# Kernel tuning notes

Measured on AMD Instinct MI355X. Metric: run time of the kernel, lower is better.

Reference implementation:

```python
import jax, jax.numpy as jnp
import numpy as np

DIM = 2048
N_HEADS = 16
N_KV_HEADS = 8
HEAD_DIM = DIM // N_HEADS  # 128
N_REP = N_HEADS // N_KV_HEADS  # 2
HIDDEN = 4 * DIM  # Project hidden dim
SEQ = 2048
BSZ = 2
ROPE_THETA = 10000.0
NEG_INF = -1e9


def setup_inputs() -> dict:
    key = jax.random.key(0)
    ks = jax.random.split(key, 10)
    s_in = 1.0 / np.sqrt(DIM)
    s_hid = 1.0 / np.sqrt(HIDDEN)
    x = jax.random.normal(ks[0], (BSZ, SEQ, DIM), jnp.float32)
    wq = jax.random.normal(ks[1], (DIM, N_HEADS * HEAD_DIM), jnp.float32) * s_in
    wk_w1 = jax.random.normal(ks[2], (DIM, HIDDEN), jnp.float32) * s_in
    wk_w2 = jax.random.normal(ks[3], (HIDDEN, N_KV_HEADS * HEAD_DIM), jnp.float32) * s_hid
    wk_w3 = jax.random.normal(ks[4], (DIM, HIDDEN), jnp.float32) * s_in
    wv_w1 = jax.random.normal(ks[5], (DIM, HIDDEN), jnp.float32) * s_in
    wv_w2 = jax.random.normal(ks[6], (HIDDEN, N_KV_HEADS * HEAD_DIM), jnp.float32) * s_hid
    wv_w3 = jax.random.normal(ks[7], (DIM, HIDDEN), jnp.float32) * s_in
    wo = jax.random.normal(ks[8], (N_HEADS * HEAD_DIM, DIM), jnp.float32) * s_in
    # RoPE tables: angle[t, j] = t * theta^(-2j/head_dim), j in [0, head_dim/2)
    inv_freq = 1.0 / (ROPE_THETA ** (np.arange(0, HEAD_DIM, 2, dtype=np.float64) / HEAD_DIM))
    ang = np.outer(np.arange(SEQ, dtype=np.float64), inv_freq)
    freqs_cos = jnp.asarray(np.cos(ang), jnp.float32)  # [SEQ, HEAD_DIM//2]
    freqs_sin = jnp.asarray(np.sin(ang), jnp.float32)
    # causal additive mask [1, 1, SEQ, SEQ]
    mask = jnp.triu(jnp.full((SEQ, SEQ), NEG_INF, jnp.float32), k=1)[None, None]
    return {
        "x": x, "wq": wq,
        "wk_w1": wk_w1, "wk_w2": wk_w2, "wk_w3": wk_w3,
        "wv_w1": wv_w1, "wv_w2": wv_w2, "wv_w3": wv_w3,
        "wo": wo, "freqs_cos": freqs_cos, "freqs_sin": freqs_sin,
        "mask": mask, "start_pos": 0,
    }


def _rope(x, cos, sin):
    # x: [b, s, h, d]; pairs (x[2j], x[2j+1]) rotated as complex multiply
    xr = x[..., 0::2]
    xi = x[..., 1::2]
    c = cos[None, :, None, :]
    s = sin[None, :, None, :]
    out_r = xr * c - xi * s
    out_i = xr * s + xi * c
    return jnp.stack([out_r, out_i], axis=-1).reshape(x.shape)


def _project(x, w1, w2, w3):
    # SwiGLU-style projection: w2(silu(x@w1) * (x@w3))
    return (jax.nn.silu(x @ w1) * (x @ w3)) @ w2


def reference(x, wq, wk_w1, wk_w2, wk_w3, wv_w1, wv_w2, wv_w3, wo,
              freqs_cos, freqs_sin, mask, start_pos):
    b, s, _ = x.shape
    q = (x @ wq).reshape(b, s, N_HEADS, HEAD_DIM)
    q = _rope(q, freqs_cos, freqs_sin)
    k = _project(x, wk_w1, wk_w2, wk_w3).reshape(b, s, N_KV_HEADS, HEAD_DIM)
    v = _project(x, wv_w1, wv_w2, wv_w3).reshape(b, s, N_KV_HEADS, HEAD_DIM)
    k = _rope(k, freqs_cos, freqs_sin)
    o_keys, o_values = k, v  # is_training=True path: cache is just current k/v
    # repeat_kv (GQA) -> [b, h, s, d]
    kr = jnp.repeat(k, N_REP, axis=2).transpose(0, 2, 1, 3)
    vr = jnp.repeat(v, N_REP, axis=2).transpose(0, 2, 1, 3)
    qt = q.transpose(0, 2, 1, 3)
    scores = jnp.einsum('bhqd,bhkd->bhqk', qt, kr) / np.sqrt(HEAD_DIM).astype(np.float32)
    scores = scores + mask
    attn = jax.nn.softmax(scores.astype(jnp.float32), axis=-1).astype(qt.dtype)
    out = jnp.einsum('bhqk,bhkd->bhqd', attn, vr)
    out = out.transpose(0, 2, 1, 3).reshape(b, s, N_HEADS * HEAD_DIM)
    return (out @ wo, o_keys, o_values)
```

## Files before the change

kernel.cpp:

```cpp
#include <hip/hip_runtime.h>

typedef unsigned short ushort_t;
typedef __attribute__((ext_vector_type(4))) float f32x4;
typedef __attribute__((ext_vector_type(8))) __bf16 bf16x8;
typedef __attribute__((ext_vector_type(4))) unsigned short ushort4_t;
typedef __attribute__((ext_vector_type(8))) unsigned short ushort8_t;
typedef __attribute__((ext_vector_type(2))) unsigned int u32x2;

#define AS1 __attribute__((address_space(1)))
#define AS3 __attribute__((address_space(3)))

__device__ __forceinline__ float bf2f(ushort_t u) {
  unsigned int v = ((unsigned int)u) << 16;
  return __builtin_bit_cast(float, v);
}
__device__ __forceinline__ ushort_t f2bf(float f) {
  unsigned int u = __builtin_bit_cast(unsigned int, f);
  u += 0x7fffu + ((u >> 16) & 1u);
  return (ushort_t)(u >> 16);
}
__device__ __forceinline__ void storeC(float* p, float v) { *p = v; }
__device__ __forceinline__ void storeC(ushort_t* p, float v) { *p = f2bf(v); }

__global__ __launch_bounds__(256) void cast_f32_bf16(const float* __restrict__ in,
                                                     ushort_t* __restrict__ outp) {
  size_t i = ((size_t)blockIdx.x * 256 + threadIdx.x) * 4;
  f32x4 v = *(const f32x4*)(const void*)&in[i];
  ushort4_t o;
#pragma unroll
  for (int j = 0; j < 4; ++j) o[j] = f2bf(v[j]);
  *(ushort4_t*)(void*)&outp[i] = o;
}

__global__ __launch_bounds__(256) void transpose_cast_b(
    const float* __restrict__ W0, const float* __restrict__ W1,
    const float* __restrict__ W2, const float* __restrict__ W3,
    ushort_t* __restrict__ Wt, int K, int N, long long strT) {
  __shared__ float tile[32][33];
  const int z = blockIdx.z;
  const float* W = (z == 0) ? W0 : (z == 1) ? W1 : (z == 2) ? W2 : W3;
  ushort_t* out = Wt + (size_t)(strT * z);
  int n0 = blockIdx.x * 32, k0 = blockIdx.y * 32;
  int tx = threadIdx.x, ty = threadIdx.y;
#pragma unroll
  for (int i = 0; i < 4; ++i)
    tile[ty + 8 * i][tx] = W[(size_t)(k0 + ty + 8 * i) * N + n0 + tx];
  __syncthreads();
#pragma unroll
  for (int i = 0; i < 4; ++i)
    out[(size_t)(n0 + ty + 8 * i) * K + k0 + tx] = f2bf(tile[tx][ty + 8 * i]);
}

__global__ __launch_bounds__(256) void silu_mul(ushort_t* __restrict__ h1,
                                                const ushort_t* __restrict__ h3) {
  size_t i = ((size_t)blockIdx.x * 256 + threadIdx.x) * 8;
  ushort8_t a = *(const ushort8_t*)(const void*)&h1[i];
  ushort8_t b = *(const ushort8_t*)(const void*)&h3[i];
#pragma unroll
  for (int j = 0; j < 8; ++j) {
    float x = bf2f(a[j]);
    float g = x / (1.0f + __expf(-x));
    a[j] = f2bf(g * bf2f(b[j]));
  }
  *(ushort8_t*)(void*)&h1[i] = a;
}

__global__ __launch_bounds__(256) void reduce_q(const ushort_t* __restrict__ part,
                                                ushort_t* __restrict__ qb,
                                                const float* __restrict__ fc,
                                                const float* __restrict__ fs) {
  const float alpha = 0.08838834764831845f;
  int p = blockIdx.x * 256 + threadIdx.x;
  size_t e0 = (size_t)p * 8;
  int i0 = (int)((e0 & 127) >> 1);
  int s = (int)((e0 >> 11) & 2047);
  ushort8_t a = *(const ushort8_t*)(const void*)&part[e0];
  ushort8_t b = *(const ushort8_t*)(const void*)&part[e0 + 8388608];
  f32x4 c4 = *(const f32x4*)(const void*)&fc[s * 64 + i0];
  f32x4 s4 = *(const f32x4*)(const void*)&fs[s * 64 + i0];
  ushort8_t o;
#pragma unroll
  for (int j = 0; j < 4; ++j) {
    float xr = bf2f(a[2 * j]) + bf2f(b[2 * j]);
    float xi = bf2f(a[2 * j + 1]) + bf2f(b[2 * j + 1]);
    float c = c4[j] * alpha, sn = s4[j] * alpha;
    o[2 * j] = f2bf(xr * c - xi * sn);
    o[2 * j + 1] = f2bf(xr * sn + xi * c);
  }
  *(ushort8_t*)(void*)&qb[e0] = o;
}

__global__ __launch_bounds__(256) void reduce_k(const ushort_t* __restrict__ part,
                                                ushort_t* __restrict__ kb,
                                                float* __restrict__ okeys,
                                                const float* __restrict__ fc,
                                                const float* __restrict__ fs) {
  int p = blockIdx.x * 256 + threadIdx.x;
  size_t e0 = (size_t)p * 8;
  int i0 = (int)((e0 & 127) >> 1);
  int s = (int)((e0 >> 10) & 2047);
  ushort8_t a0 = *(const ushort8_t*)(const void*)&part[e0];
  ushort8_t a1 = *(const ushort8_t*)(const void*)&part[e0 + 4194304];
  ushort8_t a2 = *(const ushort8_t*)(const void*)&part[e0 + 8388608];
  ushort8_t a3 = *(const ushort8_t*)(const void*)&part[e0 + 12582912];
  f32x4 c4 = *(const f32x4*)(const void*)&fc[s * 64 + i0];
  f32x4 s4 = *(const f32x4*)(const void*)&fs[s * 64 + i0];
  ushort8_t o;
  f32x4 ov0, ov1;
#pragma unroll
  for (int j = 0; j < 4; ++j) {
    float xr = bf2f(a0[2 * j]) + bf2f(a1[2 * j]) + bf2f(a2[2 * j]) + bf2f(a3[2 * j]);
    float xi = bf2f(a0[2 * j + 1]) + bf2f(a1[2 * j + 1]) + bf2f(a2[2 * j + 1]) +
               bf2f(a3[2 * j + 1]);
    float c = c4[j], sn = s4[j];
    float orr = xr * c - xi * sn;
    float oi = xr * sn + xi * c;
    o[2 * j] = f2bf(orr);
    o[2 * j + 1] = f2bf(oi);
    if (j < 2) { ov0[2 * j] = orr; ov0[2 * j + 1] = oi; }
    else       { ov1[2 * (j - 2)] = orr; ov1[2 * (j - 2) + 1] = oi; }
  }
  *(ushort8_t*)(void*)&kb[e0] = o;
  *(f32x4*)(void*)&okeys[e0] = ov0;
  *(f32x4*)(void*)&okeys[e0 + 4] = ov1;
}

__global__ __launch_bounds__(256) void reduce_v(const ushort_t* __restrict__ part,
                                                float* __restrict__ ovals,
                                                ushort_t* __restrict__ vbT) {
  __shared__ ushort_t tile[32][33];
  int s0 = blockIdx.x * 32, d0 = blockIdx.y * 32, bk = blockIdx.z;
  int b = bk >> 3, kh = bk & 7;
  int tx = threadIdx.x, ty = threadIdx.y;
#pragma unroll
  for (int i = 0; i < 4; ++i) {
    int s = s0 + ty + 8 * i;
    size_t src = ((size_t)(b * 2048 + s)) * 1024 + kh * 128 + d0 + tx;
    float v = bf2f(part[src]) + bf2f(part[src + 4194304]) +
              bf2f(part[src + 8388608]) + bf2f(part[src + 12582912]);
    tile[ty + 8 * i][tx] = f2bf(v);
    ovals[src] = v;
  }
  __syncthreads();
#pragma unroll
  for (int i = 0; i < 4; ++i) {
    int d = d0 + ty + 8 * i;
    vbT[((size_t)bk * 128 + d) * 2048 + s0 + tx] = tile[tx][ty + 8 * i];
  }
}

__global__ __launch_bounds__(256) void reduce_wo(const float* __restrict__ part,
                                                 float* __restrict__ outp) {
  size_t i = ((size_t)blockIdx.x * 256 + threadIdx.x) * 4;
  f32x4 a = *(const f32x4*)(const void*)&part[i];
  f32x4 b = *(const f32x4*)(const void*)&part[i + 8388608];
  *(f32x4*)(void*)&outp[i] = a + b;
}

__global__ __launch_bounds__(256) void flash_attn(
    const ushort_t* __restrict__ Q, const ushort_t* __restrict__ Kg,
    const ushort_t* __restrict__ VT, ushort_t* __restrict__ O) {
  __shared__ __align__(16) char smem[81920];
  const int xp = blockIdx.x;
  const int bh = blockIdx.y;
  const int b = bh >> 4, h = bh & 15, kh = h >> 1;
  const int t = threadIdx.x, w = t >> 6, lane = t & 63;
  const int fr = lane & 15, fh = lane >> 4;
  const size_t kelem0 = ((size_t)b * 2048) * 1024 + kh * 128;
  const size_t velem0 = ((size_t)(b * 8 + kh)) * 128 * 2048;
  const size_t qrow0 = (size_t)b * 2048;

  size_t oK[4], oV[4];
#pragma unroll
  for (int qv = 0; qv < 4; ++qv) {
    int row = w * 16 + qv * 4 + (lane >> 4);
    oK[qv] = (size_t)row * 1024 + (((lane & 15) ^ (row & 7)) * 8);
    int rd = w * 32 + qv * 8 + (lane >> 3);
    oV[qv] = (size_t)rd * 2048 + (((lane & 7) ^ (rd & 7)) * 8);
  }

  auto stage = [&](int tile, int buf) {
    const size_t kc = (size_t)tile * 64 * 1024;
    const int vc = tile * 64;
    char* kd = smem + buf * 16384 + w * 4096;
    char* vd = smem + 32768 + buf * 16384 + w * 4096;
#pragma unroll
    for (int qv = 0; qv < 4; ++qv) {
      __builtin_amdgcn_global_load_lds((const AS1 void*)(Kg + kelem0 + kc + oK[qv]),
                                       (AS3 void*)(kd + qv * 1024), 16, 0, 0);
      __builtin_amdgcn_global_load_lds((const AS1 void*)(VT + velem0 + oV[qv] + vc),
                                       (AS3 void*)(vd + qv * 1024), 16, 0, 0);
    }
  };

#pragma unroll 1
  for (int ph = 0; ph < 2; ++ph) {
    const int qi = ph ? (15 - xp) : xp;
    const int qw = qi * 128 + w * 32;
    const int nt = 2 * qi + 2;

    bf16x8 qF[2][4];
#pragma unroll
    for (int qt = 0; qt < 2; ++qt)
#pragma unroll
      for (int i = 0; i < 4; ++i)
        qF[qt][i] = *(const bf16x8*)(const void*)(
            Q + (qrow0 + qw + qt * 16 + fr) * 2048 + h * 128 + i * 32 + fh * 8);

    f32x4 acco[8][2] = {};
    float mrun[2] = {-1e30f, -1e30f};
    float lrun[2] = {0.0f, 0.0f};

    stage(0, 0);
#pragma unroll 1
    for (int tt = 0; tt < nt; ++tt) {
      const int c0 = tt * 64;
      if (tt + 1 < nt) {
        stage(tt + 1, (tt + 1) & 1);
        asm volatile("s_waitcnt vmcnt(8)" ::: "memory");
      } else {
        asm volatile("s_waitcnt vmcnt(0)" ::: "memory");
      }
      __builtin_amdgcn_sched_barrier(0);
      __builtin_amdgcn_s_barrier();
      const char* KL = smem + (tt & 1) * 16384;
      const char* VL = smem + 32768 + (tt & 1) * 16384;
      char* PL = smem + 65536 + w * 4096;
      if (c0 <= qw + 31) {
        f32x4 sacc[2][4] = {};
#pragma unroll
        for (int i = 0; i < 4; ++i)
#pragma unroll
          for (int mt = 0; mt < 4; ++mt) {
            bf16x8 kf = *(const bf16x8*)(const void*)(
                KL + (mt * 16 + fr) * 256 + (((i * 4 + fh) ^ (fr & 7)) * 16));
            sacc[0][mt] = __builtin_amdgcn_mfma_f32_16x16x32_bf16(kf, qF[0][i], sacc[0][mt], 0, 0, 0);
            sacc[1][mt] = __builtin_amdgcn_mfma_f32_16x16x32_bf16(kf, qF[1][i], sacc[1][mt], 0, 0, 0);
          }
        if (c0 + 63 > qw) {
#pragma unroll
          for (int qt = 0; qt < 2; ++qt) {
            int qg = qw + qt * 16 + fr;
#pragma unroll
            for (int mt = 0; mt < 4; ++mt)
#pragma unroll
              for (int j = 0; j < 4; ++j)
                if (c0 + mt * 16 + fh * 4 + j > qg) sacc[qt][mt][j] = -1e30f;
          }
        }
#pragma unroll
        for (int qt = 0; qt < 2; ++qt) {
          float mt_ = -1e30f;
#pragma unroll
          for (int mt = 0; mt < 4; ++mt)
#pragma unroll
            for (int j = 0; j < 4; ++j) mt_ = fmaxf(mt_, sacc[qt][mt][j]);
          mt_ = fmaxf(mt_, __shfl_xor(mt_, 16, 64));
          mt_ = fmaxf(mt_, __shfl_xor(mt_, 32, 64));
          float mnew = fmaxf(mrun[qt], mt_);
          float corr = __expf(mrun[qt] - mnew);
          mrun[qt] = mnew;
          float ps = 0.0f;
          float pv[4][4];
#pragma unroll
          for (int mt = 0; mt < 4; ++mt)
#pragma unroll
            for (int j = 0; j < 4; ++j) {
              float pe = __expf(sacc[qt][mt][j] - mnew);
              pv[mt][j] = pe;
              ps += pe;
            }
          ps += __shfl_xor(ps, 16, 64);
          ps += __shfl_xor(ps, 32, 64);
          lrun[qt] = lrun[qt] * corr + ps;
#pragma unroll
          for (int mt = 0; mt < 4; ++mt) {
            unsigned int u0, u1;
            asm("v_cvt_pk_bf16_f32 %0, %1, %2" : "=v"(u0) : "v"(pv[mt][0]), "v"(pv[mt][1]));
            asm("v_cvt_pk_bf16_f32 %0, %1, %2" : "=v"(u1) : "v"(pv[mt][2]), "v"(pv[mt][3]));
            u32x2 val;
            val[0] = u0;
            val[1] = u1;
            *(u32x2*)(void*)(PL + qt * 2048 + fr * 128 +
                             (((2 * mt + (fh >> 1)) ^ (fr & 7)) * 16) + (fh & 1) * 8) = val;
          }
#pragma unroll
          for (int dt = 0; dt < 8; ++dt) acco[dt][qt] *= corr;
        }
        bf16x8 pf[2][2];
#pragma unroll
        for (int qt = 0; qt < 2; ++qt)
#pragma unroll
          for (int ks = 0; ks < 2; ++ks)
            pf[qt][ks] = *(const bf16x8*)(const void*)(
                PL + qt * 2048 + fr * 128 + (((ks * 4 + fh) ^ (fr & 7)) * 16));
#pragma unroll
        for (int dt = 0; dt < 8; ++dt)
#pragma unroll
          for (int ks = 0; ks < 2; ++ks) {
            bf16x8 vf = *(const bf16x8*)(const void*)(
                VL + (dt * 16 + fr) * 128 + (((ks * 4 + fh) ^ (fr & 7)) * 16));
            acco[dt][0] = __builtin_amdgcn_mfma_f32_16x16x32_bf16(vf, pf[0][ks], acco[dt][0], 0, 0, 0);
            acco[dt][1] = __builtin_amdgcn_mfma_f32_16x16x32_bf16(vf, pf[1][ks], acco[dt][1], 0, 0, 0);
          }
      }
      __builtin_amdgcn_s_barrier();
    }
#pragma unroll
    for (int qt = 0; qt < 2; ++qt) {
      float inv = 1.0f / lrun[qt];
      const size_t rb = (qrow0 + qw + qt * 16 + fr) * 2048 + h * 128;
#pragma unroll
      for (int dt = 0; dt < 8; ++dt) {
        ushort4_t o4;
#pragma unroll
        for (int j = 0; j < 4; ++j) o4[j] = f2bf(acco[dt][qt][j] * inv);
        *(ushort4_t*)(void*)(O + rb + dt * 16 + fh * 4) = o4;
      }
    }
  }
}

template <typename CT>
__global__ __launch_bounds__(512, 2) void gemm256(
    const ushort_t* __restrict__ A, const ushort_t* __restrict__ B,
    CT* __restrict__ C, int K, int lda, int ldb, int ldc,
    int nwgx, int nwg, long long strA, long long strB, long long strC) {
  __shared__ __align__(16) char smem[131072];
  const int bz = blockIdx.y;
  const int bid = blockIdx.x;
  const int swz = (bid & 7) * (nwg >> 3) + (bid >> 3);
  const int r0 = (swz / nwgx) * 256;
  const int c0 = (swz % nwgx) * 256;
  const int t = threadIdx.x, w = t >> 6, lane = t & 63;
  const int wm = w >> 2, wn = w & 3;
  const int fr = lane & 15, fh = lane >> 4;
  const int sl2 = (fh ^ ((fr >> 1) & 3)) << 4;
  const int ldsw = w * 1024;
  const int srow = t >> 2;
  const int scb = (t & 3) ^ ((srow >> 1) & 3);
  const int NT = K >> 5;
  const ushort_t* gA = A + strA * bz + (size_t)(r0 + srow) * lda + scb * 8;
  const ushort_t* gB = B + strB * bz + (size_t)(c0 + srow) * ldb + scb * 8;

  auto stage = [&](int tile, int h, int slot) {
    char* lp = (char*)smem + slot * 16384 + ldsw;
    __builtin_amdgcn_global_load_lds(
        (const AS1 void*)(gA + (size_t)(h * 128) * lda + tile * 32),
        (AS3 void*)lp, 16, 0, 0);
    __builtin_amdgcn_global_load_lds(
        (const AS1 void*)(gB + (size_t)(h * 128) * ldb + tile * 32),
        (AS3 void*)(lp + 8192), 16, 0, 0);
  };

  f32x4 acc[8][4] = {};

  stage(0, 0, 0); stage(0, 1, 1);
  if (NT > 1) { stage(1, 0, 2); stage(1, 1, 3); }
  if (NT > 2) { stage(2, 0, 4); stage(2, 1, 5); }
  if (NT > 2)
    asm volatile("s_waitcnt vmcnt(8)" ::: "memory");
  else if (NT > 1)
    asm volatile("s_waitcnt vmcnt(4)" ::: "memory");
  else
    asm volatile("s_waitcnt vmcnt(0)" ::: "memory");
  __builtin_amdgcn_sched_barrier(0);
  __builtin_amdgcn_s_barrier();
  __builtin_amdgcn_sched_barrier(0);

  int slA = wm;
  int slB = wn >> 1;
  int st0 = 6, st1 = 7;
  const int bQuart = 8192 + (wn & 1) * 4096;

  for (int kt = 0; kt < NT; ++kt) {
    const char* la = (const char*)smem + slA * 16384 + fr * 64 + sl2;
    const char* lb = (const char*)smem + slB * 16384 + bQuart + fr * 64 + sl2;
    bf16x8 aF[8], bF[4];
#pragma unroll
    for (int m = 0; m < 4; ++m)
      aF[m] = *(const bf16x8*)(const void*)(la + m * 1024);
#pragma unroll
    for (int n = 0; n < 4; ++n)
      bF[n] = *(const bf16x8*)(const void*)(lb + n * 1024);
#pragma unroll
    for (int m = 4; m < 8; ++m)
      aF[m] = *(const bf16x8*)(const void*)(la + m * 1024);
    if (kt + 3 < NT) { stage(kt + 3, 0, st0); stage(kt + 3, 1, st1); }
    __builtin_amdgcn_sched_barrier(0);
    __builtin_amdgcn_s_setprio(1);
#pragma unroll
    for (int m = 0; m < 4; ++m)
#pragma unroll
      for (int n = 0; n < 4; ++n)
        acc[m][n] = __builtin_amdgcn_mfma_f32_16x16x32_bf16(aF[m], bF[n], acc[m][n], 0, 0, 0);
#pragma unroll
    for (int m = 4; m < 8; ++m)
#pragma unroll
      for (int n = 0; n < 4; ++n)
        acc[m][n] = __builtin_amdgcn_mfma_f32_16x16x32_bf16(aF[m], bF[n], acc[m][n], 0, 0, 0);
    __builtin_amdgcn_s_setprio(0);
    if (kt + 1 < NT) {
      if (kt + 3 < NT)
        asm volatile("s_waitcnt vmcnt(8)" ::: "memory");
      else if (kt + 2 < NT)
        asm volatile("s_waitcnt vmcnt(4)" ::: "memory");
      else
        asm volatile("s_waitcnt vmcnt(0)" ::: "memory");
      __builtin_amdgcn_sched_barrier(0);
      __builtin_amdgcn_s_barrier();
      __builtin_amdgcn_sched_barrier(0);
    }
    slA = (slA + 2) & 7;
    slB = (slB + 2) & 7;
    st0 = (st0 + 2) & 7;
    st1 = (st1 + 2) & 7;
  }

  CT* gC = C + strC * bz;
  const int cr = r0 + wm * 128 + fh * 4;
  const int cc = c0 + wn * 64 + fr;
#pragma unroll
  for (int m = 0; m < 8; ++m)
#pragma unroll
    for (int n = 0; n < 4; ++n)
#pragma unroll
      for (int j = 0; j < 4; ++j)
        storeC(&gC[(size_t)(cr + m * 16 + j) * ldc + cc + n * 16], acc[m][n][j]);
}

extern "C" void kernel_launch(void* const* d_in, const int* in_sizes, int n_in,
                              void* d_out, int out_size, void* d_ws, size_t ws_size,
                              hipStream_t stream) {
  const float* x = (const float*)d_in[0];
  const float* wq = (const float*)d_in[1];
  const float* wk1 = (const float*)d_in[2];
  const float* wk2 = (const float*)d_in[3];
  const float* wk3 = (const float*)d_in[4];
  const float* wv1 = (const float*)d_in[5];
  const float* wv2 = (const float*)d_in[6];
  const float* wv3 = (const float*)d_in[7];
  const float* wo = (const float*)d_in[8];
  const float* fc = (const float*)d_in[9];
  const float* fs = (const float*)d_in[10];

  float* outp = (float*)d_out;
  float* okeys = outp + 8388608;
  float* ovals = outp + 12582912;

  char* p = (char*)d_ws;
  auto alloc = [&](size_t bytes) {
    char* r = p;
    p += (bytes + 255) & ~(size_t)255;
    return r;
  };
  ushort_t* xb = (ushort_t*)alloc(8388608ull * 2);
  ushort_t* w4T = (ushort_t*)alloc(4ull * 16777216 * 2);
  ushort_t* w2T = (ushort_t*)alloc(2ull * 8388608 * 2);
  ushort_t* wqoT = (ushort_t*)alloc(2ull * 4194304 * 2);
  ushort_t* qb = (ushort_t*)alloc(8388608ull * 2);
  ushort_t* kb = (ushort_t*)alloc(4194304ull * 2);
  ushort_t* vbT = (ushort_t*)alloc(4194304ull * 2);
  ushort_t* ob = (ushort_t*)alloc(8388608ull * 2);
  char* hreg = alloc(134217728ull);
  ushort_t* h1 = (ushort_t*)hreg;
  ushort_t* part16 = (ushort_t*)(hreg + 67108864);
  ushort_t* partQ16 = (ushort_t*)hreg;
  float* partWO = (float*)hreg;

  ushort_t* wk1T = w4T;
  ushort_t* wk2T = w2T;
  ushort_t* wv1T = w4T + 2ull * 16777216;
  ushort_t* wv2T = w2T + 8388608;
  ushort_t* wqT = wqoT;
  ushort_t* woT = wqoT + 4194304;

  dim3 tb(32, 8);

  cast_f32_bf16<<<8192, 256, 0, stream>>>(x, xb);
  transpose_cast_b<<<dim3(256, 64, 4), tb, 0, stream>>>(wk1, wk3, wv1, wv3, w4T,
                                                        2048, 8192, 16777216);
  transpose_cast_b<<<dim3(32, 256, 2), tb, 0, stream>>>(wk2, wv2, wk2, wv2, w2T,
                                                        8192, 1024, 8388608);
  transpose_cast_b<<<dim3(64, 64, 2), tb, 0, stream>>>(wq, wo, wq, wo, wqoT,
                                                       2048, 2048, 4194304);

  gemm256<ushort_t><<<dim3(128, 2), 512, 0, stream>>>(
      xb, wqT, partQ16, 1024, 2048, 2048, 2048, 8, 128, 1024, 1024, 8388608);
  reduce_q<<<4096, 256, 0, stream>>>(partQ16, qb, fc, fs);

  gemm256<ushort_t><<<dim3(512, 2), 512, 0, stream>>>(
      xb, wk1T, h1, 2048, 2048, 2048, 8192, 32, 512, 0, 16777216, 33554432);
  silu_mul<<<16384, 256, 0, stream>>>(h1, h1 + 33554432);
  gemm256<ushort_t><<<dim3(64, 4), 512, 0, stream>>>(
      h1, wk2T, part16, 2048, 8192, 8192, 1024, 4, 64, 2048, 2048, 4194304);
  reduce_k<<<2048, 256, 0, stream>>>(part16, kb, okeys, fc, fs);

  gemm256<ushort_t><<<dim3(512, 2), 512, 0, stream>>>(
      xb, wv1T, h1, 2048, 2048, 2048, 8192, 32, 512, 0, 16777216, 33554432);
  silu_mul<<<16384, 256, 0, stream>>>(h1, h1 + 33554432);
  gemm256<ushort_t><<<dim3(64, 4), 512, 0, stream>>>(
      h1, wv2T, part16, 2048, 8192, 8192, 1024, 4, 64, 2048, 2048, 4194304);
  reduce_v<<<dim3(64, 4, 16), tb, 0, stream>>>(part16, ovals, vbT);

  flash_attn<<<dim3(8, 32), 256, 0, stream>>>(qb, kb, vbT, ob);

  gemm256<float><<<dim3(128, 2), 512, 0, stream>>>(
      ob, woT, partWO, 1024, 2048, 2048, 2048, 8, 128, 1024, 1024, 8388608);
  reduce_wo<<<8192, 256, 0, stream>>>(partWO, outp);

  (void)in_sizes; (void)n_in; (void)out_size; (void)ws_size;
}
```

Baseline: 1.017 ms.

## Shrink GEMM tile to 128x256 with double-buffered LDS and higher occupancy

The shared GEMM kernel moves from a 256x256 tile with a 4-deep, 128KB LDS pipeline to a 128x256 tile with a simple two-buffer 48KB pipeline. Each wave now holds a 4x4 accumulator block, and launch bounds request 4 blocks per CU. Grids double to cover the smaller row tiles, and the split-K partial buffer for the K/V down-projection is moved into the transposed-weight workspace. The aim is to fit more workgroups per CU and more tiles per launch so more latency can be hidden. The cost is less data reuse per tile, a shallower prefetch, and a full vmcnt(0) wait every K step.

```diff
diff --git a/kernel.cpp b/kernel.cpp
--- a/kernel.cpp
+++ b/kernel.cpp
@@ -322,106 +322,82 @@
 }
 
 template <typename CT>
-__global__ __launch_bounds__(512, 2) void gemm256(
+__global__ __launch_bounds__(512, 4) void gemm256(
     const ushort_t* __restrict__ A, const ushort_t* __restrict__ B,
     CT* __restrict__ C, int K, int lda, int ldb, int ldc,
     int nwgx, int nwg, long long strA, long long strB, long long strC) {
-  __shared__ __align__(16) char smem[131072];
+  __shared__ __align__(16) char smem[49152];
   const int bz = blockIdx.y;
   const int bid = blockIdx.x;
   const int swz = (bid & 7) * (nwg >> 3) + (bid >> 3);
-  const int r0 = (swz / nwgx) * 256;
+  const int r0 = (swz / nwgx) * 128;
   const int c0 = (swz % nwgx) * 256;
   const int t = threadIdx.x, w = t >> 6, lane = t & 63;
   const int wm = w >> 2, wn = w & 3;
   const int fr = lane & 15, fh = lane >> 4;
   const int sl2 = (fh ^ ((fr >> 1) & 3)) << 4;
-  const int ldsw = w * 1024;
   const int srow = t >> 2;
   const int scb = (t & 3) ^ ((srow >> 1) & 3);
   const int NT = K >> 5;
   const ushort_t* gA = A + strA * bz + (size_t)(r0 + srow) * lda + scb * 8;
   const ushort_t* gB = B + strB * bz + (size_t)(c0 + srow) * ldb + scb * 8;
 
-  auto stage = [&](int tile, int h, int slot) {
-    char* lp = (char*)smem + slot * 16384 + ldsw;
+  auto stage = [&](int tile) {
+    const int buf = tile & 1;
     __builtin_amdgcn_global_load_lds(
-        (const AS1 void*)(gA + (size_t)(h * 128) * lda + tile * 32),
-        (AS3 void*)lp, 16, 0, 0);
+        (const AS1 void*)(gA + tile * 32),
+        (AS3 void*)((char*)smem + buf * 8192 + t * 16), 16, 0, 0);
     __builtin_amdgcn_global_load_lds(
-        (const AS1 void*)(gB + (size_t)(h * 128) * ldb + tile * 32),
-        (AS3 void*)(lp + 8192), 16, 0, 0);
+        (const AS1 void*)(gB + tile * 32),
+        (AS3 void*)((char*)smem + 16384 + buf * 16384 + t * 16), 16, 0, 0);
+    __builtin_amdgcn_global_load_lds(
+        (const AS1 void*)(gB + (size_t)128 * ldb + tile * 32),
+        (AS3 void*)((char*)smem + 16384 + buf * 16384 + 8192 + t * 16), 16, 0, 0);
   };
 
-  f32x4 acc[8][4] = {};
-
-  stage(0, 0, 0); stage(0, 1, 1);
-  if (NT > 1) { stage(1, 0, 2); stage(1, 1, 3); }
-  if (NT > 2) { stage(2, 0, 4); stage(2, 1, 5); }
-  if (NT > 2)
-    asm volatile("s_waitcnt vmcnt(8)" ::: "memory");
-  else if (NT > 1)
-    asm volatile("s_waitcnt vmcnt(4)" ::: "memory");
-  else
-    asm volatile("s_waitcnt vmcnt(0)" ::: "memory");
+  f32x4 acc[4][4] = {};
+
+  stage(0);
+  asm volatile("s_waitcnt vmcnt(0)" ::: "memory");
   __builtin_amdgcn_sched_barrier(0);
   __builtin_amdgcn_s_barrier();
   __builtin_amdgcn_sched_barrier(0);
 
-  int slA = wm;
-  int slB = wn >> 1;
-  int st0 = 6, st1 = 7;
-  const int bQuart = 8192 + (wn & 1) * 4096;
+  const int aBase = wm * 4096 + fr * 64 + sl2;
+  const int bBase = 16384 + wn * 4096 + fr * 64 + sl2;
 
   for (int kt = 0; kt < NT; ++kt) {
-    const char* la = (const char*)smem + slA * 16384 + fr * 64 + sl2;
-    const char* lb = (const char*)smem + slB * 16384 + bQuart + fr * 64 + sl2;
-    bf16x8 aF[8], bF[4];
+    if (kt + 1 < NT) stage(kt + 1);
+    const char* la = (const char*)smem + ((kt & 1) * 8192) + aBase;
+    const char* lb = (const char*)smem + ((kt & 1) * 16384) + bBase;
+    bf16x8 aF[4], bF[4];
 #pragma unroll
     for (int m = 0; m < 4; ++m)
       aF[m] = *(const bf16x8*)(const void*)(la + m * 1024);
 #pragma unroll
     for (int n = 0; n < 4; ++n)
       bF[n] = *(const bf16x8*)(const void*)(lb + n * 1024);
-#pragma unroll
-    for (int m = 4; m < 8; ++m)
-      aF[m] = *(const bf16x8*)(const void*)(la + m * 1024);
-    if (kt + 3 < NT) { stage(kt + 3, 0, st0); stage(kt + 3, 1, st1); }
     __builtin_amdgcn_sched_barrier(0);
     __builtin_amdgcn_s_setprio(1);
 #pragma unroll
     for (int m = 0; m < 4; ++m)
-#pragma unroll
-      for (int n = 0; n < 4; ++n)
-        acc[m][n] = __builtin_amdgcn_mfma_f32_16x16x32_bf16(aF[m], bF[n], acc[m][n], 0, 0, 0);
-#pragma unroll
-    for (int m = 4; m < 8; ++m)
 #pragma unroll
       for (int n = 0; n < 4; ++n)
         acc[m][n] = __builtin_amdgcn_mfma_f32_16x16x32_bf16(aF[m], bF[n], acc[m][n], 0, 0, 0);
     __builtin_amdgcn_s_setprio(0);
     if (kt + 1 < NT) {
-      if (kt + 3 < NT)
-        asm volatile("s_waitcnt vmcnt(8)" ::: "memory");
-      else if (kt + 2 < NT)
-        asm volatile("s_waitcnt vmcnt(4)" ::: "memory");
-      else
-        asm volatile("s_waitcnt vmcnt(0)" ::: "memory");
+      asm volatile("s_waitcnt vmcnt(0)" ::: "memory");
       __builtin_amdgcn_sched_barrier(0);
       __builtin_amdgcn_s_barrier();
       __builtin_amdgcn_sched_barrier(0);
     }
-    slA = (slA + 2) & 7;
-    slB = (slB + 2) & 7;
-    st0 = (st0 + 2) & 7;
-    st1 = (st1 + 2) & 7;
   }
 
   CT* gC = C + strC * bz;
-  const int cr = r0 + wm * 128 + fh * 4;
+  const int cr = r0 + wm * 64 + fh * 4;
   const int cc = c0 + wn * 64 + fr;
 #pragma unroll
-  for (int m = 0; m < 8; ++m)
+  for (int m = 0; m < 4; ++m)
 #pragma unroll
     for (int n = 0; n < 4; ++n)
 #pragma unroll
@@ -464,9 +440,9 @@
   ushort_t* ob = (ushort_t*)alloc(8388608ull * 2);
   char* hreg = alloc(134217728ull);
   ushort_t* h1 = (ushort_t*)hreg;
-  ushort_t* part16 = (ushort_t*)(hreg + 67108864);
   ushort_t* partQ16 = (ushort_t*)hreg;
   float* partWO = (float*)hreg;
+  ushort_t* part16 = (ushort_t*)w4T;
 
   ushort_t* wk1T = w4T;
   ushort_t* wk2T = w2T;
@@ -485,28 +461,28 @@
   transpose_cast_b<<<dim3(64, 64, 2), tb, 0, stream>>>(wq, wo, wq, wo, wqoT,
                                                        2048, 2048, 4194304);
 
-  gemm256<ushort_t><<<dim3(128, 2), 512, 0, stream>>>(
-      xb, wqT, partQ16, 1024, 2048, 2048, 2048, 8, 128, 1024, 1024, 8388608);
+  gemm256<ushort_t><<<dim3(256, 2), 512, 0, stream>>>(
+      xb, wqT, partQ16, 1024, 2048, 2048, 2048, 8, 256, 1024, 1024, 8388608);
   reduce_q<<<4096, 256, 0, stream>>>(partQ16, qb, fc, fs);
 
-  gemm256<ushort_t><<<dim3(512, 2), 512, 0, stream>>>(
-      xb, wk1T, h1, 2048, 2048, 2048, 8192, 32, 512, 0, 16777216, 33554432);
+  gemm256<ushort_t><<<dim3(1024, 2), 512, 0, stream>>>(
+      xb, wk1T, h1, 2048, 2048, 2048, 8192, 32, 1024, 0, 16777216, 33554432);
   silu_mul<<<16384, 256, 0, stream>>>(h1, h1 + 33554432);
-  gemm256<ushort_t><<<dim3(64, 4), 512, 0, stream>>>(
-      h1, wk2T, part16, 2048, 8192, 8192, 1024, 4, 64, 2048, 2048, 4194304);
+  gemm256<ushort_t><<<dim3(128, 4), 512, 0, stream>>>(
+      h1, wk2T, part16, 2048, 8192, 8192, 1024, 4, 128, 2048, 2048, 4194304);
   reduce_k<<<2048, 256, 0, stream>>>(part16, kb, okeys, fc, fs);
 
-  gemm256<ushort_t><<<dim3(512, 2), 512, 0, stream>>>(
-      xb, wv1T, h1, 2048, 2048, 2048, 8192, 32, 512, 0, 16777216, 33554432);
+  gemm256<ushort_t><<<dim3(1024, 2), 512, 0, stream>>>(
+      xb, wv1T, h1, 2048, 2048, 2048, 8192, 32, 1024, 0, 16777216, 33554432);
   silu_mul<<<16384, 256, 0, stream>>>(h1, h1 + 33554432);
-  gemm256<ushort_t><<<dim3(64, 4), 512, 0, stream>>>(
-      h1, wv2T, part16, 2048, 8192, 8192, 1024, 4, 64, 2048, 2048, 4194304);
+  gemm256<ushort_t><<<dim3(128, 4), 512, 0, stream>>>(
+      h1, wv2T, part16, 2048, 8192, 8192, 1024, 4, 128, 2048, 2048, 4194304);
   reduce_v<<<dim3(64, 4, 16), tb, 0, stream>>>(part16, ovals, vbT);
 
   flash_attn<<<dim3(8, 32), 256, 0, stream>>>(qb, kb, vbT, ob);
 
-  gemm256<float><<<dim3(128, 2), 512, 0, stream>>>(
-      ob, woT, partWO, 1024, 2048, 2048, 2048, 8, 128, 1024, 1024, 8388608);
+  gemm256<float><<<dim3(256, 2), 512, 0, stream>>>(
+      ob, woT, partWO, 1024, 2048, 2048, 2048, 8, 256, 1024, 1024, 8388608);
   reduce_wo<<<8192, 256, 0, stream>>>(partWO, outp);
 
   (void)in_sizes; (void)n_in; (void)out_size; (void)ws_size;
```

New measurement: 1.091 ms. 7.3% more time.
